# Optimization experiments

Measured on AMD Instinct MI355X. Metric: run time of the kernel, lower is better.

The kernel has to match this reference:

```python
import jax, jax.numpy as jnp
import numpy as np

B, CIN, COUT, K, H, W, STYLE_DIM = 16, 128, 128, 3, 128, 128, 512

def setup_inputs() -> dict:
    key = jax.random.key(0)
    k1, k2, k3, k4 = jax.random.split(key, 4)
    x = jax.random.normal(k1, (B, CIN, H, W), dtype=jnp.float32)
    style = jax.random.normal(k2, (B, STYLE_DIM), dtype=jnp.float32)
    weight = jax.random.normal(k3, (COUT, CIN, K, K), dtype=jnp.float32)
    mod_w = jax.random.normal(k4, (CIN, STYLE_DIM), dtype=jnp.float32)
    mod_b = jnp.ones((CIN,), dtype=jnp.float32)  # EqualLinear bias_init=1
    return {"x": x, "style": style, "weight": weight, "mod_w": mod_w, "mod_b": mod_b}

def reference(x, style, weight, mod_w, mod_b):
    b, cin, h, w = x.shape
    cout, _, k, _ = weight.shape
    scale = 1.0 / np.sqrt(cin * k * k)        # conv equalized-lr scale
    lin_scale = 1.0 / np.sqrt(mod_w.shape[1])  # EqualLinear scale (lr_mul=1)
    pad = k // 2
    # affine modulation: EqualLinear(style_dim -> in_channels), bias_init=1
    s = style @ (mod_w * lin_scale).T + mod_b               # [B, Cin]
    # per-sample modulated weights
    wmod = scale * weight[None] * s[:, None, :, None, None]  # [B, Cout, Cin, k, k]
    demod = jax.lax.rsqrt(jnp.sum(wmod * wmod, axis=(2, 3, 4)) + 1e-8)  # [B, Cout]
    wmod = wmod * demod[:, :, None, None, None]
    # grouped conv with groups=batch == vmapped per-sample conv
    def conv_one(xi, wi):
        return jax.lax.conv_general_dilated(
            xi[None], wi, window_strides=(1, 1), padding=[(pad, pad), (pad, pad)],
            dimension_numbers=("NCHW", "OIHW", "NCHW"))[0]
    out = jax.vmap(conv_one)(x, wmod)  # [B, Cout, H, W]
    return out
```

## Files before the change

### kernel.cpp

```cpp
#include <hip/hip_runtime.h>
#include <hip/hip_bf16.h>


typedef __attribute__((ext_vector_type(8))) short short8;
typedef __attribute__((ext_vector_type(4))) float f32x4;

#define XPITCH (130 * 128)
#define CONV_SCALE 0.029462782549439483f
#define LIN_SCALE 0.04419417382415922f

__device__ __forceinline__ void async16(unsigned short* lds, const unsigned short* g) {
  __builtin_amdgcn_global_load_lds((const __attribute__((address_space(1))) void*)g,
                                   (__attribute__((address_space(3))) void*)lds, 16, 0, 0);
}

__device__ __forceinline__ unsigned int pack2bf(float a, float b) {
  unsigned short ha = __builtin_bit_cast(unsigned short, __float2bfloat16(a));
  unsigned short hb = __builtin_bit_cast(unsigned short, __float2bfloat16(b));
  return (unsigned int)ha | ((unsigned int)hb << 16);
}

__global__ void style_kernel(const float* __restrict__ style, const float* __restrict__ mod_w,
                             const float* __restrict__ mod_b, float* __restrict__ s_ws) {
  const int gw = blockIdx.x * 4 + (threadIdx.x >> 6);
  const int b = gw >> 7, cin = gw & 127, lane = threadIdx.x & 63;
  const float4 s0 = *(const float4*)(style + (size_t)b * 512 + lane * 4);
  const float4 s1 = *(const float4*)(style + (size_t)b * 512 + 256 + lane * 4);
  const float4 w0 = *(const float4*)(mod_w + (size_t)cin * 512 + lane * 4);
  const float4 w1 = *(const float4*)(mod_w + (size_t)cin * 512 + 256 + lane * 4);
  float acc = s0.x * w0.x + s0.y * w0.y + s0.z * w0.z + s0.w * w0.w +
              s1.x * w1.x + s1.y * w1.y + s1.z * w1.z + s1.w * w1.w;
#pragma unroll
  for (int off = 32; off; off >>= 1) acc += __shfl_xor(acc, off);
  if (lane == 0) s_ws[b * 128 + cin] = acc * LIN_SCALE + mod_b[cin];
}

__global__ void modw_kernel(const float* __restrict__ weight, const float* __restrict__ s_ws,
                            unsigned short* __restrict__ w_ws) {
  const int bid = blockIdx.x;
  const int b = bid >> 7, cout = bid & 127;
  const int cin = threadIdx.x;
  const float sv = s_ws[b * 128 + cin] * CONV_SCALE;
  const float* wp = weight + ((size_t)cout * 128 + cin) * 9;
  float v[9];
  float ss = 0.f;
#pragma unroll
  for (int j = 0; j < 9; ++j) { v[j] = wp[j] * sv; ss += v[j] * v[j]; }
#pragma unroll
  for (int off = 32; off; off >>= 1) ss += __shfl_down(ss, off);
  __shared__ float red[2];
  if ((threadIdx.x & 63) == 0) red[threadIdx.x >> 6] = ss;
  __syncthreads();
  const float dem = rsqrtf(red[0] + red[1] + 1e-8f);
#pragma unroll
  for (int j = 0; j < 9; ++j) {
    __hip_bfloat16 h = __float2bfloat16(v[j] * dem);
    w_ws[(((size_t)b * 9 + j) * 128 + cout) * 128 + cin] =
        __builtin_bit_cast(unsigned short, h);
  }
}

__global__ __launch_bounds__(256) void nhwc_kernel(const float* __restrict__ x,
                                                   unsigned short* __restrict__ xp) {
  __shared__ unsigned short T[128 * 128];
  const int bid = blockIdx.x;
  const int b = bid >> 7, y = bid & 127;
  const int tid = threadIdx.x;
  const float* xb = x + (size_t)b * (128 * 16384) + y * 128;
  unsigned short* ob = xp + (size_t)(b * 128 + y) * XPITCH;

  const int xc4 = tid & 31;
  const int cing = tid >> 5;
#pragma unroll
  for (int r = 0; r < 4; ++r) {
    const int cin0 = r * 32 + cing * 4;
    const int g = cin0 >> 2;
    float4 f[4];
#pragma unroll
    for (int j = 0; j < 4; ++j)
      f[j] = *(const float4*)(xb + (size_t)(cin0 + j) * 16384 + xc4 * 4);
#pragma unroll
    for (int i = 0; i < 4; ++i) {
      const int xc = xc4 * 4 + i;
      const int gp = g ^ (xc & 31);
      uint2 col;
      col.x = pack2bf(((const float*)&f[0])[i], ((const float*)&f[1])[i]);
      col.y = pack2bf(((const float*)&f[2])[i], ((const float*)&f[3])[i]);
      *(uint2*)(&T[xc * 128 + gp * 4]) = col;
    }
  }
  __syncthreads();
#pragma unroll
  for (int rr = 0; rr < 8; ++rr) {
    const int v = rr * 256 + tid;
    const int cg = v & 15;
    const int xc = v >> 4;
    const int s5 = xc & 31;
    const int g0 = (cg * 2) ^ s5, g1 = (cg * 2 + 1) ^ s5;
    const uint2 a = *(const uint2*)(&T[xc * 128 + g0 * 4]);
    const uint2 c = *(const uint2*)(&T[xc * 128 + g1 * 4]);
    uint4 o;
    o.x = a.x; o.y = a.y; o.z = c.x; o.w = c.y;
    *(uint4*)(ob + (xc + 1) * 128 + cg * 8) = o;
  }
  const uint4 z = {0u, 0u, 0u, 0u};
  if (tid < 16) *(uint4*)(ob + tid * 8) = z;
  else if (tid < 32) *(uint4*)(ob + 129 * 128 + (tid - 16) * 8) = z;
}

__global__ __launch_bounds__(256, 3) void conv_kernel(const unsigned short* __restrict__ xp,
                                                      const unsigned short* __restrict__ wws,
                                                      float* __restrict__ out) {
  __shared__ unsigned short lA[128 * 64];
  __shared__ unsigned short lB[128 * 64];
  const int tid = threadIdx.x;
  const int bid = (blockIdx.x & 7) * 256 + (blockIdx.x >> 3);
  const int b = bid >> 7, y = bid & 127;
  const int lane = tid & 63, w = tid >> 6;
  const int wm = w & 1, wn = w >> 1;
  const int l15 = lane & 15, q = lane >> 4;

  f32x4 acc[4][4];
#pragma unroll
  for (int i = 0; i < 4; ++i)
#pragma unroll
    for (int t = 0; t < 4; ++t) acc[i][t] = (f32x4){0.f, 0.f, 0.f, 0.f};

  const unsigned short* xb = xp + (size_t)b * 128 * XPITCH;
  const unsigned short* wb = wws + (size_t)b * 9 * 128 * 128;

  const int mbase = tid >> 3;
  const int goff = (((tid & 7) ^ ((tid >> 3) & 7)) << 3);
  const int eoff = tid * 8;

  for (int j3 = 0; j3 < 9; ++j3) {
    const int ky = j3 / 3;
    const int kx = j3 - ky * 3;
    const int yy = y + ky - 1;
    if (yy < 0 || yy > 127) continue;
    const unsigned short* Ab = wb + j3 * (128 * 128);
    const unsigned short* Bb = xb + yy * XPITCH + kx * 128;
    for (int c0 = 0; c0 < 128; c0 += 64) {
      __syncthreads();
#pragma unroll
      for (int p = 0; p < 4; ++p) {
        const int gofs = p * 4096 + mbase * 128 + c0 + goff;
        const int e = p * 2048 + eoff;
        async16(lA + e, Ab + gofs);
        async16(lB + e, Bb + gofs);
      }
      __syncthreads();
#pragma unroll
      for (int s = 0; s < 2; ++s) {
        const int axor = (((s * 4 + q) ^ (l15 & 7)) << 3);
        short8 af[4], bf[4];
#pragma unroll
        for (int i = 0; i < 4; ++i)
          af[i] = *(const short8*)(lA + (wm * 64 + i * 16 + l15) * 64 + axor);
#pragma unroll
        for (int t = 0; t < 4; ++t)
          bf[t] = *(const short8*)(lB + (wn * 64 + t * 16 + l15) * 64 + axor);
#pragma unroll
        for (int i = 0; i < 4; ++i)
#pragma unroll
          for (int t = 0; t < 4; ++t)
            acc[i][t] = __builtin_amdgcn_mfma_f32_16x16x32_bf16(af[i], bf[t], acc[i][t], 0, 0, 0);
      }
    }
  }

  float* ob = out + ((size_t)b * 128 * 128 + y) * 128;
#pragma unroll
  for (int i = 0; i < 4; ++i) {
    const int coutb = wm * 64 + i * 16 + q * 4;
#pragma unroll
    for (int r = 0; r < 4; ++r) {
      float* orow = ob + (size_t)(coutb + r) * (128 * 128);
#pragma unroll
      for (int t = 0; t < 4; ++t) orow[wn * 64 + t * 16 + l15] = acc[i][t][r];
    }
  }
}

extern "C" void kernel_launch(void* const* d_in, const int* in_sizes, int n_in,
                              void* d_out, int out_size, void* d_ws, size_t ws_size,
                              hipStream_t stream) {
  const float* x = (const float*)d_in[0];
  const float* style = (const float*)d_in[1];
  const float* weight = (const float*)d_in[2];
  const float* mod_w = (const float*)d_in[3];
  const float* mod_b = (const float*)d_in[4];
  float* out = (float*)d_out;

  char* ws = (char*)d_ws;
  float* s_ws = (float*)ws;
  unsigned short* w_ws = (unsigned short*)(ws + 8192);
  unsigned short* xp = (unsigned short*)(ws + (8u << 20));

  style_kernel<<<512, 256, 0, stream>>>(style, mod_w, mod_b, s_ws);
  modw_kernel<<<16 * 128, 128, 0, stream>>>(weight, s_ws, w_ws);
  nhwc_kernel<<<16 * 128, 256, 0, stream>>>(x, xp);
  conv_kernel<<<16 * 128, 256, 0, stream>>>(xp, w_ws, out);
}
```

Measured before the change: 317.0 us.

## Fuse NCHW-to-bf16 transpose into conv kernel, staging three input rows in LDS

Removes the separate nhwc transpose kernel and its padded bf16 workspace. Each conv block now reads fp32 input rows directly, converts them to bf16 and transposes them through LDS into a three-row buffer. All 3x3 taps then reuse that buffer, and zeroed fragments handle the x-boundary. This saves the intermediate write and read plus a kernel launch. In exchange each input row is read and converted about three times across blocks, more LDS is used per block, and occupancy drops to 2 blocks per CU.

```diff
diff --git a/kernel.cpp b/kernel.cpp
--- a/kernel.cpp
+++ b/kernel.cpp
@@ -5,7 +5,6 @@
 typedef __attribute__((ext_vector_type(8))) short short8;
 typedef __attribute__((ext_vector_type(4))) float f32x4;
 
-#define XPITCH (130 * 128)
 #define CONV_SCALE 0.029462782549439483f
 #define LIN_SCALE 0.04419417382415922f
 
@@ -60,59 +59,12 @@
   }
 }
 
-__global__ __launch_bounds__(256) void nhwc_kernel(const float* __restrict__ x,
-                                                   unsigned short* __restrict__ xp) {
-  __shared__ unsigned short T[128 * 128];
-  const int bid = blockIdx.x;
-  const int b = bid >> 7, y = bid & 127;
-  const int tid = threadIdx.x;
-  const float* xb = x + (size_t)b * (128 * 16384) + y * 128;
-  unsigned short* ob = xp + (size_t)(b * 128 + y) * XPITCH;
-
-  const int xc4 = tid & 31;
-  const int cing = tid >> 5;
-#pragma unroll
-  for (int r = 0; r < 4; ++r) {
-    const int cin0 = r * 32 + cing * 4;
-    const int g = cin0 >> 2;
-    float4 f[4];
-#pragma unroll
-    for (int j = 0; j < 4; ++j)
-      f[j] = *(const float4*)(xb + (size_t)(cin0 + j) * 16384 + xc4 * 4);
-#pragma unroll
-    for (int i = 0; i < 4; ++i) {
-      const int xc = xc4 * 4 + i;
-      const int gp = g ^ (xc & 31);
-      uint2 col;
-      col.x = pack2bf(((const float*)&f[0])[i], ((const float*)&f[1])[i]);
-      col.y = pack2bf(((const float*)&f[2])[i], ((const float*)&f[3])[i]);
-      *(uint2*)(&T[xc * 128 + gp * 4]) = col;
-    }
-  }
-  __syncthreads();
-#pragma unroll
-  for (int rr = 0; rr < 8; ++rr) {
-    const int v = rr * 256 + tid;
-    const int cg = v & 15;
-    const int xc = v >> 4;
-    const int s5 = xc & 31;
-    const int g0 = (cg * 2) ^ s5, g1 = (cg * 2 + 1) ^ s5;
-    const uint2 a = *(const uint2*)(&T[xc * 128 + g0 * 4]);
-    const uint2 c = *(const uint2*)(&T[xc * 128 + g1 * 4]);
-    uint4 o;
-    o.x = a.x; o.y = a.y; o.z = c.x; o.w = c.y;
-    *(uint4*)(ob + (xc + 1) * 128 + cg * 8) = o;
-  }
-  const uint4 z = {0u, 0u, 0u, 0u};
-  if (tid < 16) *(uint4*)(ob + tid * 8) = z;
-  else if (tid < 32) *(uint4*)(ob + 129 * 128 + (tid - 16) * 8) = z;
-}
-
-__global__ __launch_bounds__(256, 3) void conv_kernel(const unsigned short* __restrict__ xp,
+__global__ __launch_bounds__(256, 2) void conv_kernel(const float* __restrict__ x,
                                                       const unsigned short* __restrict__ wws,
                                                       float* __restrict__ out) {
+  __shared__ unsigned short xr[3 * 128 * 64];
   __shared__ unsigned short lA[128 * 64];
-  __shared__ unsigned short lB[128 * 64];
+
   const int tid = threadIdx.x;
   const int bid = (blockIdx.x & 7) * 256 + (blockIdx.x >> 3);
   const int b = bid >> 7, y = bid & 127;
@@ -126,40 +78,92 @@
 #pragma unroll
     for (int t = 0; t < 4; ++t) acc[i][t] = (f32x4){0.f, 0.f, 0.f, 0.f};
 
-  const unsigned short* xb = xp + (size_t)b * 128 * XPITCH;
+  const float* xb = x + (size_t)b * (128 * 16384);
   const unsigned short* wb = wws + (size_t)b * 9 * 128 * 128;
 
   const int mbase = tid >> 3;
   const int goff = (((tid & 7) ^ ((tid >> 3) & 7)) << 3);
   const int eoff = tid * 8;
 
-  for (int j3 = 0; j3 < 9; ++j3) {
-    const int ky = j3 / 3;
-    const int kx = j3 - ky * 3;
-    const int yy = y + ky - 1;
-    if (yy < 0 || yy > 127) continue;
-    const unsigned short* Ab = wb + j3 * (128 * 128);
-    const unsigned short* Bb = xb + yy * XPITCH + kx * 128;
-    for (int c0 = 0; c0 < 128; c0 += 64) {
-      __syncthreads();
-#pragma unroll
-      for (int p = 0; p < 4; ++p) {
-        const int gofs = p * 4096 + mbase * 128 + c0 + goff;
-        const int e = p * 2048 + eoff;
-        async16(lA + e, Ab + gofs);
-        async16(lB + e, Bb + gofs);
+  const int xq = tid & 31, cq8 = tid >> 5;
+  const int tg16 = tid & 7, txr = tid >> 3;
+
+  int nt[4];
+#pragma unroll
+  for (int t = 0; t < 4; ++t) nt[t] = wn * 64 + t * 16 + l15;
+
+  const short8 zero8 = {0, 0, 0, 0, 0, 0, 0, 0};
+
+  for (int c0 = 0; c0 < 128; c0 += 64) {
+#pragma unroll
+    for (int r3 = 0; r3 < 3; ++r3) {
+      const int yy = y + r3 - 1;
+      if (yy < 0 || yy > 127) continue;
+      __syncthreads();
+      const float* xrow = xb + (size_t)c0 * 16384 + (size_t)yy * 128;
+      float4 f[2][4];
+#pragma unroll
+      for (int rr = 0; rr < 2; ++rr)
+#pragma unroll
+        for (int j = 0; j < 4; ++j)
+          f[rr][j] = *(const float4*)(xrow + (size_t)(rr * 32 + cq8 * 4 + j) * 16384 + xq * 4);
+#pragma unroll
+      for (int rr = 0; rr < 2; ++rr) {
+        const int g8 = rr * 8 + cq8;
+#pragma unroll
+        for (int i = 0; i < 4; ++i) {
+          const int xp = xq * 4 + i;
+          const int gp = g8 ^ (xp & 15);
+          uint2 col;
+          col.x = pack2bf(((const float*)&f[rr][0])[i], ((const float*)&f[rr][1])[i]);
+          col.y = pack2bf(((const float*)&f[rr][2])[i], ((const float*)&f[rr][3])[i]);
+          *(uint2*)(lA + xp * 64 + gp * 4) = col;
+        }
       }
       __syncthreads();
 #pragma unroll
+      for (int rr = 0; rr < 4; ++rr) {
+        const int xp = rr * 32 + txr;
+        const int s15 = xp & 15;
+        const int gp0 = (tg16 * 2) ^ s15, gp1 = (tg16 * 2 + 1) ^ s15;
+        const uint2 a = *(const uint2*)(lA + xp * 64 + gp0 * 4);
+        const uint2 c = *(const uint2*)(lA + xp * 64 + gp1 * 4);
+        uint4 o;
+        o.x = a.x; o.y = a.y; o.z = c.x; o.w = c.y;
+        *(uint4*)(xr + r3 * 8192 + xp * 64 + ((tg16 ^ (xp & 7)) << 3)) = o;
+      }
+    }
+
+    for (int j3 = 0; j3 < 9; ++j3) {
+      const int ky = j3 / 3, kx = j3 - ky * 3;
+      const int yy = y + ky - 1;
+      if (yy < 0 || yy > 127) continue;
+      __syncthreads();
+#pragma unroll
+      for (int p = 0; p < 4; ++p)
+        async16(lA + p * 2048 + eoff, wb + j3 * 16384 + c0 + p * 4096 + mbase * 128 + goff);
+      int xcb[4];
+#pragma unroll
+      for (int t = 0; t < 4; ++t) xcb[t] = nt[t] + (kx - 1);
+      const bool lo = (xcb[0] < 0);
+      const bool hi = (xcb[3] > 127);
+      if (lo) xcb[0] = 0;
+      if (hi) xcb[3] = 127;
+      const unsigned short* xkr = xr + ky * 8192;
+      __syncthreads();
+#pragma unroll
       for (int s = 0; s < 2; ++s) {
-        const int axor = (((s * 4 + q) ^ (l15 & 7)) << 3);
+        const int s4q = s * 4 + q;
+        const int axor = ((s4q ^ (l15 & 7)) << 3);
         short8 af[4], bf[4];
 #pragma unroll
         for (int i = 0; i < 4; ++i)
           af[i] = *(const short8*)(lA + (wm * 64 + i * 16 + l15) * 64 + axor);
 #pragma unroll
         for (int t = 0; t < 4; ++t)
-          bf[t] = *(const short8*)(lB + (wn * 64 + t * 16 + l15) * 64 + axor);
+          bf[t] = *(const short8*)(xkr + xcb[t] * 64 + ((s4q ^ (xcb[t] & 7)) << 3));
+        if (lo) bf[0] = zero8;
+        if (hi) bf[3] = zero8;
 #pragma unroll
         for (int i = 0; i < 4; ++i)
 #pragma unroll
@@ -195,10 +199,8 @@
   char* ws = (char*)d_ws;
   float* s_ws = (float*)ws;
   unsigned short* w_ws = (unsigned short*)(ws + 8192);
-  unsigned short* xp = (unsigned short*)(ws + (8u << 20));
 
   style_kernel<<<512, 256, 0, stream>>>(style, mod_w, mod_b, s_ws);
   modw_kernel<<<16 * 128, 128, 0, stream>>>(weight, s_ws, w_ws);
-  nhwc_kernel<<<16 * 128, 256, 0, stream>>>(x, xp);
-  conv_kernel<<<16 * 128, 256, 0, stream>>>(xp, w_ws, out);
-}
+  conv_kernel<<<16 * 128, 256, 0, stream>>>(x, w_ws, out);
+}
```

Result: faster. 307.3 us (-3.1%).

## Double-buffer conv K-loop, two output rows per 512-thread block, padded rows

Applied to the files above, without the earlier changes.

The conv kernel now computes two output rows per block with 512 threads, sharing each loaded weight tile across both rows. It double-buffers LDS with async global-to-LDS loads of the next K step, overlapped with the MFMA work on the current one, using explicit vmcnt waits and raised priority around the MFMA block. The NHWC transform now writes zero top and bottom halo rows, so the conv loop no longer has to branch on boundary rows. In exchange LDS use grows to about 96 KB per block, and the boundary rows now do redundant MFMA work on zeros.

```diff
diff --git a/kernel.cpp b/kernel.cpp
--- a/kernel.cpp
+++ b/kernel.cpp
@@ -62,12 +62,17 @@
 
 __global__ __launch_bounds__(256) void nhwc_kernel(const float* __restrict__ x,
                                                    unsigned short* __restrict__ xp) {
+  const int b = blockIdx.y, row = blockIdx.x;
+  const int tid = threadIdx.x;
+  unsigned short* ob = xp + ((size_t)b * 130 + row) * XPITCH;
+  if (row == 0 || row == 129) {
+    const uint4 z = {0u, 0u, 0u, 0u};
+    for (int v = tid; v < 1040; v += 256) ((uint4*)ob)[v] = z;
+    return;
+  }
+  const int y = row - 1;
   __shared__ unsigned short T[128 * 128];
-  const int bid = blockIdx.x;
-  const int b = bid >> 7, y = bid & 127;
-  const int tid = threadIdx.x;
   const float* xb = x + (size_t)b * (128 * 16384) + y * 128;
-  unsigned short* ob = xp + (size_t)(b * 128 + y) * XPITCH;
 
   const int xc4 = tid & 31;
   const int cing = tid >> 5;
@@ -108,14 +113,15 @@
   else if (tid < 32) *(uint4*)(ob + 129 * 128 + (tid - 16) * 8) = z;
 }
 
-__global__ __launch_bounds__(256, 3) void conv_kernel(const unsigned short* __restrict__ xp,
+__global__ __launch_bounds__(512, 2) void conv_kernel(const unsigned short* __restrict__ xp,
                                                       const unsigned short* __restrict__ wws,
                                                       float* __restrict__ out) {
-  __shared__ unsigned short lA[128 * 64];
-  __shared__ unsigned short lB[128 * 64];
+  __shared__ unsigned short lA[2][128 * 64];
+  __shared__ unsigned short lB[2][256 * 64];
+
   const int tid = threadIdx.x;
-  const int bid = (blockIdx.x & 7) * 256 + (blockIdx.x >> 3);
-  const int b = bid >> 7, y = bid & 127;
+  const int bid = (blockIdx.x & 7) * 128 + (blockIdx.x >> 3);
+  const int b = bid >> 6, y0 = (bid & 63) * 2;
   const int lane = tid & 63, w = tid >> 6;
   const int wm = w & 1, wn = w >> 1;
   const int l15 = lane & 15, q = lane >> 4;
@@ -126,58 +132,83 @@
 #pragma unroll
     for (int t = 0; t < 4; ++t) acc[i][t] = (f32x4){0.f, 0.f, 0.f, 0.f};
 
-  const unsigned short* xb = xp + (size_t)b * 128 * XPITCH;
+  const unsigned short* xpb = xp + (size_t)b * 130 * XPITCH;
   const unsigned short* wb = wws + (size_t)b * 9 * 128 * 128;
 
-  const int mbase = tid >> 3;
-  const int goff = (((tid & 7) ^ ((tid >> 3) & 7)) << 3);
-  const int eoff = tid * 8;
-
-  for (int j3 = 0; j3 < 9; ++j3) {
-    const int ky = j3 / 3;
-    const int kx = j3 - ky * 3;
-    const int yy = y + ky - 1;
-    if (yy < 0 || yy > 127) continue;
-    const unsigned short* Ab = wb + j3 * (128 * 128);
-    const unsigned short* Bb = xb + yy * XPITCH + kx * 128;
-    for (int c0 = 0; c0 < 128; c0 += 64) {
-      __syncthreads();
-#pragma unroll
-      for (int p = 0; p < 4; ++p) {
-        const int gofs = p * 4096 + mbase * 128 + c0 + goff;
-        const int e = p * 2048 + eoff;
-        async16(lA + e, Ab + gofs);
-        async16(lB + e, Bb + gofs);
-      }
-      __syncthreads();
-#pragma unroll
-      for (int s = 0; s < 2; ++s) {
-        const int axor = (((s * 4 + q) ^ (l15 & 7)) << 3);
-        short8 af[4], bf[4];
-#pragma unroll
-        for (int i = 0; i < 4; ++i)
-          af[i] = *(const short8*)(lA + (wm * 64 + i * 16 + l15) * 64 + axor);
-#pragma unroll
-        for (int t = 0; t < 4; ++t)
-          bf[t] = *(const short8*)(lB + (wn * 64 + t * 16 + l15) * 64 + axor);
-#pragma unroll
-        for (int i = 0; i < 4; ++i)
-#pragma unroll
-          for (int t = 0; t < 4; ++t)
-            acc[i][t] = __builtin_amdgcn_mfma_f32_16x16x32_bf16(af[i], bf[t], acc[i][t], 0, 0, 0);
-      }
-    }
-  }
-
-  float* ob = out + ((size_t)b * 128 * 128 + y) * 128;
+  const int am = tid >> 3;
+  const unsigned short* asrc = wb + am * 128 + (((tid & 7) ^ (am & 7)) << 3);
+  const unsigned short* bsrc[4];
+#pragma unroll
+  for (int p = 0; p < 4; ++p) {
+    const int g = p * 512 + tid, n = g >> 3;
+    const int c16 = (g & 7) ^ (n & 7);
+    bsrc[p] = xpb + (size_t)(y0 + (n >> 7)) * XPITCH + (n & 127) * 128 + (c16 << 3);
+  }
+  const int dst8 = tid * 8;
+
+#define STAGE_STEP(cur_, j3_, ky_, kx_, c0_)                         \
+  do {                                                               \
+    const int ka = (j3_) * 16384 + (c0_);                            \
+    async16(lA[cur_] + dst8, asrc + ka);                             \
+    async16(lA[cur_] + 4096 + dst8, asrc + ka + 8192);               \
+    const int kb = (ky_)*XPITCH + (kx_)*128 + (c0_);                 \
+    async16(lB[cur_] + dst8, bsrc[0] + kb);                          \
+    async16(lB[cur_] + 4096 + dst8, bsrc[1] + kb);                   \
+    async16(lB[cur_] + 8192 + dst8, bsrc[2] + kb);                   \
+    async16(lB[cur_] + 12288 + dst8, bsrc[3] + kb);                  \
+  } while (0)
+
+  STAGE_STEP(0, 0, 0, 0, 0);
+
+#pragma unroll
+  for (int t = 0; t < 18; ++t) {
+    const int cur = t & 1;
+    if (t < 17) {
+      const int tn = t + 1;
+      const int j3n = tn >> 1, c0n = (tn & 1) << 6;
+      const int kyn = j3n / 3, kxn = j3n % 3;
+      STAGE_STEP(cur ^ 1, j3n, kyn, kxn, c0n);
+      asm volatile("s_waitcnt vmcnt(6)" ::: "memory");
+    } else {
+      asm volatile("s_waitcnt vmcnt(0)" ::: "memory");
+    }
+    asm volatile("s_barrier" ::: "memory");
+
+    short8 af[2][4], bf[2][4];
+#pragma unroll
+    for (int s = 0; s < 2; ++s) {
+      const int axor = (((s * 4 + q) ^ (l15 & 7)) << 3);
+#pragma unroll
+      for (int i = 0; i < 4; ++i)
+        af[s][i] = *(const short8*)(&lA[cur][(wm * 64 + i * 16 + l15) * 64 + axor]);
+#pragma unroll
+      for (int i = 0; i < 4; ++i)
+        bf[s][i] = *(const short8*)(&lB[cur][(wn * 64 + i * 16 + l15) * 64 + axor]);
+    }
+    asm volatile("s_waitcnt lgkmcnt(0)" ::: "memory");
+    __builtin_amdgcn_sched_barrier(0);
+    __builtin_amdgcn_s_setprio(1);
+#pragma unroll
+    for (int s = 0; s < 2; ++s)
+#pragma unroll
+      for (int i = 0; i < 4; ++i)
+#pragma unroll
+        for (int u = 0; u < 4; ++u)
+          acc[i][u] = __builtin_amdgcn_mfma_f32_16x16x32_bf16(af[s][i], bf[s][u], acc[i][u], 0, 0, 0);
+    __builtin_amdgcn_s_setprio(0);
+    asm volatile("s_barrier" ::: "memory");
+  }
+#undef STAGE_STEP
+
+  float* obase = out + (size_t)b * (128 * 16384) + (y0 + (wn >> 1)) * 128 + (wn & 1) * 64;
 #pragma unroll
   for (int i = 0; i < 4; ++i) {
     const int coutb = wm * 64 + i * 16 + q * 4;
 #pragma unroll
-    for (int r = 0; r < 4; ++r) {
-      float* orow = ob + (size_t)(coutb + r) * (128 * 128);
-#pragma unroll
-      for (int t = 0; t < 4; ++t) orow[wn * 64 + t * 16 + l15] = acc[i][t][r];
+    for (int rr = 0; rr < 4; ++rr) {
+      float* orow = obase + (size_t)(coutb + rr) * 16384;
+#pragma unroll
+      for (int t = 0; t < 4; ++t) orow[t * 16 + l15] = acc[i][t][rr];
     }
   }
 }
@@ -195,10 +226,10 @@
   char* ws = (char*)d_ws;
   float* s_ws = (float*)ws;
   unsigned short* w_ws = (unsigned short*)(ws + 8192);
-  unsigned short* xp = (unsigned short*)(ws + (8u << 20));
+  unsigned short* xp = (unsigned short*)(ws + (5u << 20));
 
   style_kernel<<<512, 256, 0, stream>>>(style, mod_w, mod_b, s_ws);
   modw_kernel<<<16 * 128, 128, 0, stream>>>(weight, s_ws, w_ws);
-  nhwc_kernel<<<16 * 128, 256, 0, stream>>>(x, xp);
-  conv_kernel<<<16 * 128, 256, 0, stream>>>(xp, w_ws, out);
-}
+  nhwc_kernel<<<dim3(130, 16), 256, 0, stream>>>(x, xp);
+  conv_kernel<<<16 * 64, 512, 0, stream>>>(xp, w_ws, out);
+}
```

After: 348.1 us. 1.1x slower.
